# Performance work log

Hardware: AMD Instinct MI355X
Metric: run time of the kernel (lower is better)

Reference implementation:

```python
import jax, jax.numpy as jnp
import numpy as np

D_IN, D_K, D_V, BLOCK = 1024, 64, 64, 2048
B, T = 4, 2048

def setup_inputs() -> dict:
    key = jax.random.key(0)
    k0, k1, k2, k3 = jax.random.split(key, 4)
    x = jax.random.normal(k0, (B, T, D_IN), dtype=jnp.float32)
    s = 1.0 / np.sqrt(D_IN)
    Wq = jax.random.normal(k1, (D_IN, D_K), dtype=jnp.float32) * s
    Wk = jax.random.normal(k2, (D_IN, D_K), dtype=jnp.float32) * s
    Wv = jax.random.normal(k3, (D_IN, D_V), dtype=jnp.float32) * s
    return {"x": x, "Wq": Wq, "Wk": Wk, "Wv": Wv}

def reference(x, Wq, Wk, Wv):
    # Q,K,V projections (Linear without bias)
    Q = jnp.einsum('btc,ck->btk', x, Wq)
    K = jnp.einsum('btc,ck->btk', x, Wk)
    V = jnp.einsum('btc,cv->btv', x, Wv)
    Tq = x.shape[1]
    scores = jnp.einsum('bqk,btk->bqt', Q, K)  # [B,T,T]
    causal = jnp.tril(jnp.ones((Tq, Tq), dtype=bool))
    scores = jnp.where(causal, scores, -jnp.inf)
    attn = jax.nn.softmax(scores, axis=-1)
    # NOTE: original divides the AV product by sqrt(d_k) AFTER softmax
    out = jnp.einsum('bqt,btv->bqv', attn, V) / jnp.sqrt(jnp.asarray(K.shape[-1], dtype=x.dtype))
    return out
```

## Files before the change

kernel.cpp:

```cpp
#include <hip/hip_runtime.h>
#include <math.h>

typedef unsigned short u16;
typedef __attribute__((ext_vector_type(4))) float f32x4;
typedef __bf16 bf16x8 __attribute__((ext_vector_type(8)));

#define MFMA16(a,b,c) __builtin_amdgcn_mfma_f32_16x16x32_bf16((a),(b),(c),0,0,0)

typedef const __attribute__((address_space(1))) unsigned GU;
typedef __attribute__((address_space(3))) unsigned LU;
__device__ __forceinline__ void gl_lds16(const void* g, void* l) {
    __builtin_amdgcn_global_load_lds((GU*)g, (LU*)l, 16, 0, 0);
}

__device__ __forceinline__ u16 f2b(float f) {
    __bf16 h = (__bf16)f;
    return __builtin_bit_cast(u16, h);
}
__device__ __forceinline__ float b2f(u16 u) {
    unsigned v = (unsigned)u << 16;
    return __builtin_bit_cast(float, v);
}

__global__ __launch_bounds__(128) void wtrans_kernel(
    const float* __restrict__ Wq, const float* __restrict__ Wk,
    const float* __restrict__ Wv, u16* __restrict__ Wt2)
{
    const int n = blockIdx.x;
    const float* W = (n < 64) ? Wq : ((n < 128) ? Wk : Wv);
    const int nc = n & 63, cg = n >> 4, r = n & 15;
    const int t = threadIdx.x;
    const int k0 = t * 8;
    const int kstep = k0 >> 6, kh = (k0 >> 5) & 1, kg = (k0 >> 3) & 3;
    u16 hh[8], ll[8];
#pragma unroll
    for (int i = 0; i < 8; ++i) {
        const float a = W[(size_t)(k0 + i) * 64 + nc];
        hh[i] = f2b(a);
        ll[i] = f2b(a - b2f(hh[i]));
    }
    const size_t fi = (((size_t)kstep * 12 + cg) * 2 + kh) * 2;
    u16* dst = Wt2 + fi * 512 + kg * 128 + r * 8;
    uint4 vh, vl;
    vh.x = (uint)hh[0] | ((uint)hh[1] << 16); vh.y = (uint)hh[2] | ((uint)hh[3] << 16);
    vh.z = (uint)hh[4] | ((uint)hh[5] << 16); vh.w = (uint)hh[6] | ((uint)hh[7] << 16);
    vl.x = (uint)ll[0] | ((uint)ll[1] << 16); vl.y = (uint)ll[2] | ((uint)ll[3] << 16);
    vl.z = (uint)ll[4] | ((uint)ll[5] << 16); vl.w = (uint)ll[6] | ((uint)ll[7] << 16);
    *(uint4*)dst         = vh;
    *(uint4*)(dst + 512) = vl;
}

__global__ __launch_bounds__(256, 2) void proj_kernel(
    const float* __restrict__ x, const u16* __restrict__ Wt2,
    u16* __restrict__ Qhi, u16* __restrict__ Qlo,
    u16* __restrict__ Khi, u16* __restrict__ Klo, u16* __restrict__ Vt)
{
    __shared__ u16 WB[2][12288];
    __shared__ u16 vs[32][72];

    const int t = threadIdx.x, w = t >> 6, lane = t & 63;
    const int lo = lane & 15, hi = lane >> 4;
    const int rt = blockIdx.x >> 1, nh = blockIdx.x & 1;
    const int row0 = rt * 32;
    const int mh = w >> 1, nt = w & 1;

    f32x4 acc[3];
#pragma unroll
    for (int i = 0; i < 3; ++i) acc[i] = (f32x4){0.f, 0.f, 0.f, 0.f};

    const float* xrow = x + (size_t)(row0 + mh * 16 + lo) * 1024 + hi * 8;

    auto stage = [&](int buf, int step) {
        const u16* src = Wt2 + (size_t)step * 24576 + (size_t)nh * 12288
                             + (size_t)(w * 6) * 512 + (size_t)lane * 8;
        u16* dst = &WB[buf][(w * 6) * 512];
#pragma unroll
        for (int i = 0; i < 6; ++i)
            gl_lds16(src + i * 512, dst + i * 512);
    };
    auto loadXf = [&](float4 (&xv)[2][2], int step) {
#pragma unroll
        for (int kh = 0; kh < 2; ++kh) {
            xv[kh][0] = *(const float4*)(xrow + step * 64 + kh * 32);
            xv[kh][1] = *(const float4*)(xrow + step * 64 + kh * 32 + 4);
        }
    };
    auto compute = [&](int buf, const float4 (&xv)[2][2]) {
        bf16x8 ah[2], al[2];
#pragma unroll
        for (int kh = 0; kh < 2; ++kh)
#pragma unroll
            for (int j = 0; j < 2; ++j)
#pragma unroll
                for (int c = 0; c < 4; ++c) {
                    const float f = (&xv[kh][j].x)[c];
                    const __bf16 h = (__bf16)f;
                    ah[kh][j * 4 + c] = h;
                    al[kh][j * 4 + c] = (__bf16)(f - (float)h);
                }
        const char* base = (const char*)&WB[buf][0];
#pragma unroll
        for (int i = 0; i < 3; ++i) {
            const int lc = nt * 3 + i;
#pragma unroll
            for (int kh = 0; kh < 2; ++kh) {
                const int fb = ((lc * 2 + kh) * 2) * 1024;
                const bf16x8 wh = *(const bf16x8*)(base + fb + lane * 16);
                const bf16x8 wl = *(const bf16x8*)(base + fb + 1024 + lane * 16);
                acc[i] = MFMA16(ah[kh], wh, acc[i]);
                acc[i] = MFMA16(ah[kh], wl, acc[i]);
                acc[i] = MFMA16(al[kh], wh, acc[i]);
            }
        }
    };

    float4 xA[2][2], xB[2][2];
    stage(0, 0);
    loadXf(xA, 0);
    __syncthreads();
    int buf = 0;
    for (int step = 0; step < 16; ++step) {
        if (step < 15) { stage(buf ^ 1, step + 1); loadXf(xB, step + 1); }
        compute(buf, xA);
        __syncthreads();
        if (step < 15) {
#pragma unroll
            for (int kh = 0; kh < 2; ++kh) { xA[kh][0] = xB[kh][0]; xA[kh][1] = xB[kh][1]; }
        }
        buf ^= 1;
    }

#pragma unroll
    for (int i = 0; i < 3; ++i) {
        const int cg = nh * 6 + nt * 3 + i;
#pragma unroll
        for (int r = 0; r < 4; ++r) {
            const float v = acc[i][r];
            const int row = row0 + mh * 16 + hi * 4 + r;
            const u16 h = f2b(v);
            if (cg < 4) {
                Qhi[(size_t)row * 64 + cg * 16 + lo] = h;
                Qlo[(size_t)row * 64 + cg * 16 + lo] = f2b(v - b2f(h));
            } else if (cg < 8) {
                Khi[(size_t)row * 64 + (cg - 4) * 16 + lo] = h;
                Klo[(size_t)row * 64 + (cg - 4) * 16 + lo] = f2b(v - b2f(h));
            } else {
                vs[mh * 16 + hi * 4 + r][(cg - 8) * 16 + lo] = h;
            }
        }
    }
    __syncthreads();
    if (nh == 1) {
        const int bb = row0 >> 11, tok0 = row0 & 2047;
        const int d = t >> 2, part = t & 3;
        u16 tmp[8];
#pragma unroll
        for (int i = 0; i < 8; ++i) tmp[i] = vs[part * 8 + i][d];
        uint4 v4;
        v4.x = (uint)tmp[0] | ((uint)tmp[1] << 16);
        v4.y = (uint)tmp[2] | ((uint)tmp[3] << 16);
        v4.z = (uint)tmp[4] | ((uint)tmp[5] << 16);
        v4.w = (uint)tmp[6] | ((uint)tmp[7] << 16);
        *(uint4*)(Vt + (size_t)bb * 131072 + (size_t)d * 2048 + tok0 + part * 8) = v4;
    }
}

__global__ __launch_bounds__(512, 2) void attn_kernel(
    const u16* __restrict__ Qhi, const u16* __restrict__ Qlo,
    const u16* __restrict__ Khi, const u16* __restrict__ Klo,
    const u16* __restrict__ Vt, float* __restrict__ out)
{
    __shared__ u16 P[8][16 * 64];
    __shared__ float OA[8][16][64];
    __shared__ float LS[8][16];

    const int pi = blockIdx.x, b = blockIdx.y;
    const int t = threadIdx.x, w = t >> 6, l = t & 63;
    const int lo = l & 15, hi = l >> 4;

    const u16* Qh = Qhi + (size_t)b * 131072;
    const u16* Ql = Qlo + (size_t)b * 131072;
    const u16* Kh = Khi + (size_t)b * 131072;
    const u16* Kl = Klo + (size_t)b * 131072;
    const u16* V  = Vt  + (size_t)b * 131072;

    u16* Pw = P[w];

#pragma unroll 1
    for (int phase = 0; phase < 2; ++phase) {
        const int p = phase ? pi : (127 - pi);
        const int q0 = p * 16;
        const int nt = (p >> 2) + 1;

        bf16x8 aqh[2], aql[2];
#pragma unroll
        for (int s = 0; s < 2; ++s) {
            aqh[s] = *(const bf16x8*)(Qh + (size_t)(q0 + lo) * 64 + s * 32 + hi * 8);
            aql[s] = *(const bf16x8*)(Ql + (size_t)(q0 + lo) * 64 + s * 32 + hi * 8);
        }

        f32x4 acc[4];
        float ls[4];
#pragma unroll
        for (int r = 0; r < 4; ++r) { acc[r] = (f32x4){0.f,0.f,0.f,0.f}; ls[r] = 0.f; }

        bf16x8 kh[4][2], kl[4][2];
        auto loadK = [&](int j0) {
#pragma unroll
            for (int kg = 0; kg < 4; ++kg)
#pragma unroll
                for (int s = 0; s < 2; ++s) {
                    const size_t off = (size_t)(j0 + kg * 16 + lo) * 64 + s * 32 + hi * 8;
                    kh[kg][s] = *(const bf16x8*)(Kh + off);
                    kl[kg][s] = *(const bf16x8*)(Kl + off);
                }
        };

        if (w < nt) loadK(w * 64);
#pragma unroll 1
        for (int j = w; j < nt; j += 8) {
            const int j0 = j * 64;
            bf16x8 bv[4][2];
#pragma unroll
            for (int dg = 0; dg < 4; ++dg)
#pragma unroll
                for (int s = 0; s < 2; ++s)
                    bv[dg][s] = *(const bf16x8*)(V + (size_t)(dg * 16 + lo) * 2048 + j0 + s * 32 + hi * 8);

            f32x4 S[4];
            const f32x4 zf = (f32x4){0.f,0.f,0.f,0.f};
#pragma unroll
            for (int kg = 0; kg < 4; ++kg) {
                f32x4 sv = zf;
                sv = MFMA16(aqh[0], kh[kg][0], sv);
                sv = MFMA16(aqh[1], kh[kg][1], sv);
                sv = MFMA16(aqh[0], kl[kg][0], sv);
                sv = MFMA16(aqh[1], kl[kg][1], sv);
                sv = MFMA16(aql[0], kh[kg][0], sv);
                sv = MFMA16(aql[1], kh[kg][1], sv);
                S[kg] = sv;
            }

            if (j + 8 < nt) loadK((j + 8) * 64);

            const bool dm = (j == nt - 1);
#pragma unroll
            for (int r = 0; r < 4; ++r) {
                const int row = q0 + hi * 4 + r;
                float sv0 = S[0][r], sv1 = S[1][r], sv2 = S[2][r], sv3 = S[3][r];
                if (dm) {
                    sv0 = (j0 +      lo > row) ? -INFINITY : sv0;
                    sv1 = (j0 + 16 + lo > row) ? -INFINITY : sv1;
                    sv2 = (j0 + 32 + lo > row) ? -INFINITY : sv2;
                    sv3 = (j0 + 48 + lo > row) ? -INFINITY : sv3;
                }
                const u16 u0 = f2b(__expf(sv0)), u1 = f2b(__expf(sv1));
                const u16 u2 = f2b(__expf(sv2)), u3 = f2b(__expf(sv3));
                float ps = b2f(u0) + b2f(u1) + b2f(u2) + b2f(u3);
#pragma unroll
                for (int msk = 8; msk; msk >>= 1) ps += __shfl_xor(ps, msk, 64);
                ls[r] += ps;
                const int rowL = hi * 4 + r;
                const int base = rowL * 64;
                const int sw = rowL & 7;
                Pw[base + (((0 + (lo >> 3)) ^ sw) << 3) + (lo & 7)] = u0;
                Pw[base + (((2 + (lo >> 3)) ^ sw) << 3) + (lo & 7)] = u1;
                Pw[base + (((4 + (lo >> 3)) ^ sw) << 3) + (lo & 7)] = u2;
                Pw[base + (((6 + (lo >> 3)) ^ sw) << 3) + (lo & 7)] = u3;
            }
            const bf16x8 pa0 = *(const bf16x8*)&Pw[lo * 64 + (((hi    ) ^ (lo & 7)) << 3)];
            const bf16x8 pa1 = *(const bf16x8*)&Pw[lo * 64 + (((hi + 4) ^ (lo & 7)) << 3)];
#pragma unroll
            for (int dg = 0; dg < 4; ++dg) {
                acc[dg] = MFMA16(pa0, bv[dg][0], acc[dg]);
                acc[dg] = MFMA16(pa1, bv[dg][1], acc[dg]);
            }
        }

#pragma unroll
        for (int r = 0; r < 4; ++r) {
            if (lo == 0) LS[w][hi * 4 + r] = ls[r];
#pragma unroll
            for (int dg = 0; dg < 4; ++dg) OA[w][hi * 4 + r][dg * 16 + lo] = acc[dg][r];
        }
        __syncthreads();

        {
            const int row = t >> 5, c0 = (t & 31) * 2;
            float s0 = 0.f, s1 = 0.f, Lt = 0.f;
#pragma unroll
            for (int wv = 0; wv < 8; ++wv) {
                s0 += OA[wv][row][c0];
                s1 += OA[wv][row][c0 + 1];
                Lt += LS[wv][row];
            }
            const float inv = 0.125f / Lt;
            float2 o = make_float2(s0 * inv, s1 * inv);
            *(float2*)(out + ((size_t)b * 2048 + q0 + row) * 64 + c0) = o;
        }
        __syncthreads();
    }
}

extern "C" void kernel_launch(void* const* d_in, const int* in_sizes, int n_in,
                              void* d_out, int out_size, void* d_ws, size_t ws_size,
                              hipStream_t stream) {
    const float* x  = (const float*)d_in[0];
    const float* Wq = (const float*)d_in[1];
    const float* Wk = (const float*)d_in[2];
    const float* Wv = (const float*)d_in[3];
    float* outp = (float*)d_out;

    u16* Wt2 = (u16*)d_ws;
    u16* Qhi = Wt2 + 393216;
    u16* Qlo = Qhi + 524288;
    u16* Khi = Qlo + 524288;
    u16* Klo = Khi + 524288;
    u16* Vt  = Klo + 524288;

    wtrans_kernel<<<dim3(192), dim3(128), 0, stream>>>(Wq, Wk, Wv, Wt2);
    proj_kernel<<<dim3(512), dim3(256), 0, stream>>>(x, Wt2, Qhi, Qlo, Khi, Klo, Vt);
    attn_kernel<<<dim3(64, 4), dim3(512), 0, stream>>>(Qhi, Qlo, Khi, Klo, Vt, outp);
}
```

Before: 67.73 us.

## Restructure projection kernel with per-wave triple-buffered pipeline and full N per block

The projection kernel now computes all 192 output columns for 32 rows per block (256 blocks instead of 512), with each wave owning three column groups and two row groups. Each wave stages its own weight slice through a private triple-buffered LDS ring using direct global-to-LDS loads and a three-deep register prefetch of x. Ordering uses explicit vmcnt/lgkmcnt waits via inline asm instead of block-wide __syncthreads. This removes the duplicate x reads and barrier stalls, but it halves the grid, increases register pressure, and relies on hand-tuned wait counts being correct.

```diff
diff --git a/kernel.cpp b/kernel.cpp
--- a/kernel.cpp
+++ b/kernel.cpp
@@ -2,7 +2,9 @@
 #include <math.h>
 
 typedef unsigned short u16;
+typedef unsigned int uint32;
 typedef __attribute__((ext_vector_type(4))) float f32x4;
+typedef __attribute__((ext_vector_type(4))) unsigned int u32x4;
 typedef __bf16 bf16x8 __attribute__((ext_vector_type(8)));
 
 #define MFMA16(a,b,c) __builtin_amdgcn_mfma_f32_16x16x32_bf16((a),(b),(c),0,0,0)
@@ -21,6 +23,17 @@
     unsigned v = (unsigned)u << 16;
     return __builtin_bit_cast(float, v);
 }
+
+__device__ __forceinline__ void agload4(f32x4& d, const float* p) {
+    asm volatile("global_load_dwordx4 %0, %1, off" : "=&v"(d) : "v"(p) : "memory");
+}
+__device__ __forceinline__ void dsr(bf16x8& d, uint32 a) {
+    u32x4 tmp;
+    asm volatile("ds_read_b128 %0, %1" : "=&v"(tmp) : "v"(a) : "memory");
+    d = __builtin_bit_cast(bf16x8, tmp);
+}
+#define WAITVM_I(n) asm volatile("s_waitcnt vmcnt(" #n ")" ::: "memory")
+#define WAITVM(n) WAITVM_I(n)
 
 __global__ __launch_bounds__(128) void wtrans_kernel(
     const float* __restrict__ Wq, const float* __restrict__ Wk,
@@ -50,93 +63,119 @@
     *(uint4*)(dst + 512) = vl;
 }
 
-__global__ __launch_bounds__(256, 2) void proj_kernel(
+__device__ __forceinline__ void stage6(const u16* __restrict__ Wt2,
+                                       u16 (&WB)[4][3][6][512],
+                                       int w, int nq, int reg, int step, int kh, int lane) {
+#pragma unroll
+    for (int i = 0; i < 3; ++i)
+#pragma unroll
+        for (int hl = 0; hl < 2; ++hl) {
+            const int fi = ((step * 12 + nq * 3 + i) * 2 + kh) * 2 + hl;
+            gl_lds16(Wt2 + (size_t)fi * 512 + lane * 8, &WB[w][reg][i * 2 + hl][0]);
+        }
+}
+__device__ __forceinline__ void issue8(f32x4 (&xs)[8], const float* r0, const float* r1, int step) {
+#pragma unroll
+    for (int kh = 0; kh < 2; ++kh)
+#pragma unroll
+        for (int j = 0; j < 2; ++j) {
+            agload4(xs[0 * 4 + kh * 2 + j], r0 + step * 64 + kh * 32 + j * 4);
+            agload4(xs[1 * 4 + kh * 2 + j], r1 + step * 64 + kh * 32 + j * 4);
+        }
+}
+__device__ __forceinline__ void conv8(bf16x8& ah, bf16x8& al, f32x4 a, f32x4 b) {
+#pragma unroll
+    for (int e = 0; e < 4; ++e) {
+        { float v = a[e]; __bf16 hb = (__bf16)v; ah[e] = hb; al[e] = (__bf16)(v - (float)hb); }
+        { float v = b[e]; __bf16 hb = (__bf16)v; ah[4 + e] = hb; al[4 + e] = (__bf16)(v - (float)hb); }
+    }
+}
+
+#define PROJ_HALF(H_, WC_)                                                          \
+    do {                                                                            \
+        if ((H_) + 2 <= 31) {                                                       \
+            stage6(Wt2, WB, w, nq, ((H_) + 2) % 3, ((H_) + 2) >> 1, ((H_) + 2) & 1, lane); \
+        }                                                                           \
+        if ((((H_) & 1) == 0) && ((H_) >> 1) + 2 <= 15) {                           \
+            issue8(xr[(((H_) >> 1) + 2) % 3], xrow0, xrow1, ((H_) >> 1) + 2);       \
+        }                                                                           \
+        WAITVM(WC_);                                                                \
+        __builtin_amdgcn_sched_barrier(0);                                          \
+        bf16x8 wh0, wl0, wh1, wl1, wh2, wl2;                                        \
+        dsr(wh0, dsa + (uint32)((((H_) % 3) * 6 + 0) * 1024));                      \
+        dsr(wl0, dsa + (uint32)((((H_) % 3) * 6 + 1) * 1024));                      \
+        dsr(wh1, dsa + (uint32)((((H_) % 3) * 6 + 2) * 1024));                      \
+        dsr(wl1, dsa + (uint32)((((H_) % 3) * 6 + 3) * 1024));                      \
+        dsr(wh2, dsa + (uint32)((((H_) % 3) * 6 + 4) * 1024));                      \
+        dsr(wl2, dsa + (uint32)((((H_) % 3) * 6 + 5) * 1024));                      \
+        asm volatile("s_waitcnt lgkmcnt(0)" ::: "memory");                          \
+        __builtin_amdgcn_sched_barrier(0);                                          \
+        _Pragma("unroll")                                                           \
+        for (int rg = 0; rg < 2; ++rg) {                                            \
+            bf16x8 ah, al;                                                          \
+            conv8(ah, al, xr[((H_) >> 1) % 3][rg * 4 + ((H_) & 1) * 2 + 0],         \
+                          xr[((H_) >> 1) % 3][rg * 4 + ((H_) & 1) * 2 + 1]);        \
+            acc[rg][0] = MFMA16(ah, wh0, acc[rg][0]);                               \
+            acc[rg][0] = MFMA16(ah, wl0, acc[rg][0]);                               \
+            acc[rg][0] = MFMA16(al, wh0, acc[rg][0]);                               \
+            acc[rg][1] = MFMA16(ah, wh1, acc[rg][1]);                               \
+            acc[rg][1] = MFMA16(ah, wl1, acc[rg][1]);                               \
+            acc[rg][1] = MFMA16(al, wh1, acc[rg][1]);                               \
+            acc[rg][2] = MFMA16(ah, wh2, acc[rg][2]);                               \
+            acc[rg][2] = MFMA16(ah, wl2, acc[rg][2]);                               \
+            acc[rg][2] = MFMA16(al, wh2, acc[rg][2]);                               \
+        }                                                                           \
+    } while (0)
+
+__global__ __launch_bounds__(256) void proj_kernel(
     const float* __restrict__ x, const u16* __restrict__ Wt2,
     u16* __restrict__ Qhi, u16* __restrict__ Qlo,
     u16* __restrict__ Khi, u16* __restrict__ Klo, u16* __restrict__ Vt)
 {
-    __shared__ u16 WB[2][12288];
+    __shared__ u16 WB[4][3][6][512];
     __shared__ u16 vs[32][72];
 
     const int t = threadIdx.x, w = t >> 6, lane = t & 63;
     const int lo = lane & 15, hi = lane >> 4;
-    const int rt = blockIdx.x >> 1, nh = blockIdx.x & 1;
-    const int row0 = rt * 32;
-    const int mh = w >> 1, nt = w & 1;
-
-    f32x4 acc[3];
-#pragma unroll
-    for (int i = 0; i < 3; ++i) acc[i] = (f32x4){0.f, 0.f, 0.f, 0.f};
-
-    const float* xrow = x + (size_t)(row0 + mh * 16 + lo) * 1024 + hi * 8;
-
-    auto stage = [&](int buf, int step) {
-        const u16* src = Wt2 + (size_t)step * 24576 + (size_t)nh * 12288
-                             + (size_t)(w * 6) * 512 + (size_t)lane * 8;
-        u16* dst = &WB[buf][(w * 6) * 512];
-#pragma unroll
-        for (int i = 0; i < 6; ++i)
-            gl_lds16(src + i * 512, dst + i * 512);
-    };
-    auto loadXf = [&](float4 (&xv)[2][2], int step) {
-#pragma unroll
-        for (int kh = 0; kh < 2; ++kh) {
-            xv[kh][0] = *(const float4*)(xrow + step * 64 + kh * 32);
-            xv[kh][1] = *(const float4*)(xrow + step * 64 + kh * 32 + 4);
-        }
-    };
-    auto compute = [&](int buf, const float4 (&xv)[2][2]) {
-        bf16x8 ah[2], al[2];
-#pragma unroll
-        for (int kh = 0; kh < 2; ++kh)
-#pragma unroll
-            for (int j = 0; j < 2; ++j)
-#pragma unroll
-                for (int c = 0; c < 4; ++c) {
-                    const float f = (&xv[kh][j].x)[c];
-                    const __bf16 h = (__bf16)f;
-                    ah[kh][j * 4 + c] = h;
-                    al[kh][j * 4 + c] = (__bf16)(f - (float)h);
-                }
-        const char* base = (const char*)&WB[buf][0];
-#pragma unroll
-        for (int i = 0; i < 3; ++i) {
-            const int lc = nt * 3 + i;
-#pragma unroll
-            for (int kh = 0; kh < 2; ++kh) {
-                const int fb = ((lc * 2 + kh) * 2) * 1024;
-                const bf16x8 wh = *(const bf16x8*)(base + fb + lane * 16);
-                const bf16x8 wl = *(const bf16x8*)(base + fb + 1024 + lane * 16);
-                acc[i] = MFMA16(ah[kh], wh, acc[i]);
-                acc[i] = MFMA16(ah[kh], wl, acc[i]);
-                acc[i] = MFMA16(al[kh], wh, acc[i]);
-            }
-        }
-    };
-
-    float4 xA[2][2], xB[2][2];
-    stage(0, 0);
-    loadXf(xA, 0);
-    __syncthreads();
-    int buf = 0;
-    for (int step = 0; step < 16; ++step) {
-        if (step < 15) { stage(buf ^ 1, step + 1); loadXf(xB, step + 1); }
-        compute(buf, xA);
-        __syncthreads();
-        if (step < 15) {
-#pragma unroll
-            for (int kh = 0; kh < 2; ++kh) { xA[kh][0] = xB[kh][0]; xA[kh][1] = xB[kh][1]; }
-        }
-        buf ^= 1;
-    }
-
+    const int nq = w;
+    const int row0 = blockIdx.x * 32;
+
+    f32x4 acc[2][3];
+#pragma unroll
+    for (int rg = 0; rg < 2; ++rg)
+#pragma unroll
+        for (int i = 0; i < 3; ++i) acc[rg][i] = (f32x4){0.f, 0.f, 0.f, 0.f};
+
+    const float* xrow0 = x + (size_t)(row0 + lo) * 1024 + hi * 8;
+    const float* xrow1 = x + (size_t)(row0 + 16 + lo) * 1024 + hi * 8;
+    const uint32 wbase = (uint32)(size_t)(LU*)(&WB[w][0][0][0]);
+    const uint32 dsa = wbase + (uint32)lane * 16u;
+
+    f32x4 xr[3][8];
+
+    stage6(Wt2, WB, w, nq, 0, 0, 0, lane);
+    issue8(xr[0], xrow0, xrow1, 0);
+    stage6(Wt2, WB, w, nq, 1, 0, 1, lane);
+    issue8(xr[1], xrow0, xrow1, 1);
+
+    PROJ_HALF(0, 28);  PROJ_HALF(1, 20);  PROJ_HALF(2, 28);  PROJ_HALF(3, 20);
+    PROJ_HALF(4, 28);  PROJ_HALF(5, 20);  PROJ_HALF(6, 28);  PROJ_HALF(7, 20);
+    PROJ_HALF(8, 28);  PROJ_HALF(9, 20);  PROJ_HALF(10, 28); PROJ_HALF(11, 20);
+    PROJ_HALF(12, 28); PROJ_HALF(13, 20); PROJ_HALF(14, 28); PROJ_HALF(15, 20);
+    PROJ_HALF(16, 28); PROJ_HALF(17, 20); PROJ_HALF(18, 28); PROJ_HALF(19, 20);
+    PROJ_HALF(20, 28); PROJ_HALF(21, 20); PROJ_HALF(22, 28); PROJ_HALF(23, 20);
+    PROJ_HALF(24, 28); PROJ_HALF(25, 20); PROJ_HALF(26, 28); PROJ_HALF(27, 20);
+    PROJ_HALF(28, 20); PROJ_HALF(29, 12); PROJ_HALF(30, 6);  PROJ_HALF(31, 0);
+
+#pragma unroll
+    for (int rg = 0; rg < 2; ++rg)
 #pragma unroll
     for (int i = 0; i < 3; ++i) {
-        const int cg = nh * 6 + nt * 3 + i;
+        const int cg = nq * 3 + i;
 #pragma unroll
         for (int r = 0; r < 4; ++r) {
-            const float v = acc[i][r];
-            const int row = row0 + mh * 16 + hi * 4 + r;
+            const float v = acc[rg][i][r];
+            const int row = row0 + rg * 16 + hi * 4 + r;
             const u16 h = f2b(v);
             if (cg < 4) {
                 Qhi[(size_t)row * 64 + cg * 16 + lo] = h;
@@ -145,12 +184,12 @@
                 Khi[(size_t)row * 64 + (cg - 4) * 16 + lo] = h;
                 Klo[(size_t)row * 64 + (cg - 4) * 16 + lo] = f2b(v - b2f(h));
             } else {
-                vs[mh * 16 + hi * 4 + r][(cg - 8) * 16 + lo] = h;
+                vs[rg * 16 + hi * 4 + r][(cg - 8) * 16 + lo] = h;
             }
         }
     }
     __syncthreads();
-    if (nh == 1) {
+    {
         const int bb = row0 >> 11, tok0 = row0 & 2047;
         const int d = t >> 2, part = t & 3;
         u16 tmp[8];
@@ -319,6 +358,6 @@
     u16* Vt  = Klo + 524288;
 
     wtrans_kernel<<<dim3(192), dim3(128), 0, stream>>>(Wq, Wk, Wv, Wt2);
-    proj_kernel<<<dim3(512), dim3(256), 0, stream>>>(x, Wt2, Qhi, Qlo, Khi, Klo, Vt);
+    proj_kernel<<<dim3(256), dim3(256), 0, stream>>>(x, Wt2, Qhi, Qlo, Khi, Klo, Vt);
     attn_kernel<<<dim3(64, 4), dim3(512), 0, stream>>>(Qhi, Qlo, Khi, Klo, Vt, outp);
 }
```

Result: faster. 63.04 us (-6.9%).
